# Performance work log

Measured on AMD Instinct MI355X. Metric: run time of the kernel, lower is better.

Reference implementation:

```python
import jax, jax.numpy as jnp
import numpy as np

Q, C, T = 256, 128, 128
L = Q + C + T            # 512
D = 1024                 # d_model
H = 8                    # heads
DK = D // H              # 128 = self_attn.d_k
F = 3                    # num_latent_relations
R = 50                   # num_relation_kinds = len(relations2id)
FF = 4 * D               # feed-forward hidden
DEFAULT_QQ_ID = 0        # relations2id['q:q-default']
EPS = 1e-5


def setup_inputs():
    key = jax.random.key(0)
    ks = jax.random.split(key, 40)
    s = 0.02
    def nrm(k, shape, scale=s):
        return jax.random.normal(k, shape, jnp.float32) * scale
    inp = {
        'x': jax.random.normal(ks[0], (1, L, D), jnp.float32),
        'qc_relation': jax.random.uniform(ks[1], (Q, C, F), jnp.float32),
        'cq_relation': jax.random.uniform(ks[2], (C, Q, F), jnp.float32),
        'qt_relation': jax.random.uniform(ks[3], (Q, T, F), jnp.float32),
        'tq_relation': jax.random.uniform(ks[4], (T, Q, F), jnp.float32),
        'ct_relation': jax.random.randint(ks[5], (C + T, C + T), 0, R, jnp.int32),
        'predefined_relation': jax.random.randint(ks[6], (L, L), 0, R, jnp.int32),
        'mask': jnp.ones((1, L, L), jnp.int32),
        # relation embedding tables
        'rel_k_emb': nrm(ks[7], (R, DK)), 'rel_v_emb': nrm(ks[8], (R, DK)),
        'lqc_k': nrm(ks[9], (F, DK)), 'lqc_v': nrm(ks[10], (F, DK)),
        'lcq_k': nrm(ks[11], (F, DK)), 'lcq_v': nrm(ks[12], (F, DK)),
        'lqt_k': nrm(ks[13], (F, DK)), 'lqt_v': nrm(ks[14], (F, DK)),
        'ltq_k': nrm(ks[15], (F, DK)), 'ltq_v': nrm(ks[16], (F, DK)),
        # attention projections (torch Linear: y = x @ W.T + b)
        'Wq': nrm(ks[17], (D, D)), 'bq': jnp.zeros((D,), jnp.float32),
        'Wk': nrm(ks[18], (D, D)), 'bk': jnp.zeros((D,), jnp.float32),
        'Wv': nrm(ks[19], (D, D)), 'bv': jnp.zeros((D,), jnp.float32),
        'Wo': nrm(ks[20], (D, D)), 'bo': jnp.zeros((D,), jnp.float32),
        # layer norms
        'ln1_g': jnp.ones((D,), jnp.float32), 'ln1_b': jnp.zeros((D,), jnp.float32),
        'ln2_g': jnp.ones((D,), jnp.float32), 'ln2_b': jnp.zeros((D,), jnp.float32),
        # FFN
        'W1': nrm(ks[21], (FF, D)), 'b1': jnp.zeros((FF,), jnp.float32),
        'W2': nrm(ks[22], (D, FF)), 'b2': jnp.zeros((D,), jnp.float32),
    }
    return inp


def layer_norm(x, g, b):
    m = jnp.mean(x, -1, keepdims=True)
    v = jnp.mean((x - m) ** 2, -1, keepdims=True)
    return (x - m) * jax.lax.rsqrt(v + EPS) * g + b


def build_latent_relation(ct, qc, cq, qt, tq, emb, lqc, lcq, lqt, ltq):
    # qq block: every entry is the default-qq embedding row
    qq = jnp.broadcast_to(emb[DEFAULT_QQ_ID], (Q, Q, DK))
    qc_e = jnp.einsum('qcf,fd->qcd', qc, lqc)
    cq_e = jnp.einsum('cqf,fd->cqd', cq, lcq)
    qt_e = jnp.einsum('qtf,fd->qtd', qt, lqt)
    tq_e = jnp.einsum('tqf,fd->tqd', tq, ltq)
    ct_e = emb[ct]                                      # [(c+t),(c+t),DK]
    top = jnp.concatenate([qq, qc_e, qt_e], axis=1)      # [Q, L, DK]
    bot = jnp.concatenate([jnp.concatenate([cq_e, tq_e], 0), ct_e], axis=1)  # [C+T, L, DK]
    return jnp.concatenate([top, bot], axis=0)           # [L, L, DK]


def relation_attention(x, rel_k, rel_v, mask, Wq, bq, Wk, bk, Wv, bv, Wo, bo):
    B = x.shape[0]
    def proj(W, b):
        return (x @ W.T + b).reshape(B, L, H, DK).transpose(0, 2, 1, 3)  # [B,H,L,DK]
    q, k, v = proj(Wq, bq), proj(Wk, bk), proj(Wv, bv)
    scores = (jnp.einsum('bhid,bhjd->bhij', q, k)
              + jnp.einsum('bhid,ijd->bhij', q, rel_k)) / jnp.sqrt(jnp.float32(DK))
    scores = jnp.where(mask[:, None] == 0, jnp.float32(-1e9), scores)
    p = jax.nn.softmax(scores, axis=-1)
    o = (jnp.einsum('bhij,bhjd->bhid', p, v)
         + jnp.einsum('bhij,ijd->bhid', p, rel_v))
    o = o.transpose(0, 2, 1, 3).reshape(B, L, D)
    return o @ Wo.T + bo


def reference(x, qc_relation, cq_relation, qt_relation, tq_relation,
              ct_relation, predefined_relation, mask,
              rel_k_emb, rel_v_emb, lqc_k, lqc_v, lcq_k, lcq_v,
              lqt_k, lqt_v, ltq_k, ltq_v,
              Wq, bq, Wk, bk, Wv, bv, Wo, bo,
              ln1_g, ln1_b, ln2_g, ln2_b, W1, b1, W2, b2):
    # latent relation build + combine with predefined lookup
    rel_k = (rel_k_emb[predefined_relation]
             + build_latent_relation(ct_relation, qc_relation, cq_relation,
                                     qt_relation, tq_relation,
                                     rel_k_emb, lqc_k, lcq_k, lqt_k, ltq_k))
    rel_v = (rel_v_emb[predefined_relation]
             + build_latent_relation(ct_relation, qc_relation, cq_relation,
                                     qt_relation, tq_relation,
                                     rel_v_emb, lqc_v, lcq_v, lqt_v, ltq_v))
    # sublayer 0: pre-norm relation-biased self attention (dropout=0)
    h = x + relation_attention(layer_norm(x, ln1_g, ln1_b), rel_k, rel_v, mask,
                               Wq, bq, Wk, bk, Wv, bv, Wo, bo)
    # sublayer 1: pre-norm FFN
    y = layer_norm(h, ln2_g, ln2_b)
    ffn = jax.nn.relu(y @ W1.T + b1) @ W2.T + b2
    return h + ffn
```

## Files before the change

### kernel.cpp

```cpp
#include <hip/hip_runtime.h>
#include <hip/hip_bf16.h>

#define LL 512
#define DD 1024
#define HH 8
#define DKK 128
#define QQ 256
#define CCC 128
#define TTT 128
#define RR 50
#define FFF 4096
#define KLD 576
#define SLD 576

typedef __attribute__((ext_vector_type(8))) short short8;
typedef __attribute__((ext_vector_type(4))) float float4v;

__device__ __forceinline__ unsigned short f2bu(float f) {
  __hip_bfloat16 h = __float2bfloat16(f);
  unsigned short u; __builtin_memcpy(&u, &h, 2); return u;
}
__device__ __forceinline__ float b2f(unsigned short u) {
  unsigned int v = ((unsigned int)u) << 16;
  float f; __builtin_memcpy(&f, &v, 4); return f;
}
__device__ __forceinline__ int4 cvt8(float4 x, float4 y) {
  int4 o;
  o.x = (int)f2bu(x.x) | ((int)f2bu(x.y) << 16);
  o.y = (int)f2bu(x.z) | ((int)f2bu(x.w) << 16);
  o.z = (int)f2bu(y.x) | ((int)f2bu(y.y) << 16);
  o.w = (int)f2bu(y.z) | ((int)f2bu(y.w) << 16);
  return o;
}

__device__ __forceinline__ void lds_barrier() {
  __builtin_amdgcn_sched_barrier(0);
  __builtin_amdgcn_s_waitcnt(0xC07F);
  __builtin_amdgcn_s_barrier();
  __builtin_amdgcn_sched_barrier(0);
}

#define LOADSET(A0,A1,B0,B1,F0,F1,F2,F3,itv) { int k0v = (itv) << 6;          \
  A0 = *(const int4*)(Az + (size_t)(bm + r)*lda + k0v + gc*8);                \
  A1 = *(const int4*)(Az + (size_t)(bm + 32 + r)*lda + k0v + gc*8);           \
  if constexpr (!CONVB) {                                                     \
    B0 = *(const int4*)(Bz16 + (size_t)(bnb + r)*ldb + k0v + gc*8);           \
    if constexpr (NB > 1)                                                     \
      B1 = *(const int4*)(Bz16 + (size_t)(bnb + 32 + r)*ldb + k0v + gc*8);    \
  } else {                                                                    \
    F0 = *(const float4*)(Bz32 + (size_t)(bnb + r)*ldb + k0v + gc*8);         \
    F1 = *(const float4*)(Bz32 + (size_t)(bnb + r)*ldb + k0v + gc*8 + 4);     \
    if constexpr (NB > 1) {                                                   \
      F2 = *(const float4*)(Bz32 + (size_t)(bnb + 32 + r)*ldb + k0v + gc*8);  \
      F3 = *(const float4*)(Bz32 + (size_t)(bnb + 32 + r)*ldb + k0v + gc*8 + 4); } } }

#define STORESET2(basep,A0,A1,B0,B1,F0,F1,F2,F3) {                            \
  char* bse = (basep);                                                        \
  *(int4*)(bse + r*128 + sl*16) = A0;                                         \
  *(int4*)(bse + (32 + r)*128 + sl*16) = A1;                                  \
  if constexpr (!CONVB) {                                                     \
    *(int4*)(bse + ABYTES + r*128 + sl*16) = B0;                              \
    if constexpr (NB > 1)                                                     \
      *(int4*)(bse + ABYTES + (32 + r)*128 + sl*16) = B1;                     \
  } else {                                                                    \
    *(int4*)(bse + ABYTES + r*128 + sl*16) = cvt8(F0, F1);                    \
    if constexpr (NB > 1)                                                     \
      *(int4*)(bse + ABYTES + (32 + r)*128 + sl*16) = cvt8(F2, F3); } }

__global__ __launch_bounds__(256) void kprep_kernel(
    const float* __restrict__ embk,
    const float* __restrict__ lqc, const float* __restrict__ lqt,
    const float* __restrict__ lcq, const float* __restrict__ ltq,
    unsigned short* __restrict__ Kh)
{
  int g = blockIdx.x*256 + threadIdx.x;
  if (g >= 8*64*128) return;
  int d = g & 127, rr = (g >> 7) & 63, h = g >> 13;
  float v = 0.f;
  if (rr < 50) v = embk[rr*128 + d];
  else if (rr < 62) {
    int u = rr - 50; int tb = u/3, f = u - tb*3;
    const float* tab = (tb==0) ? lqc : (tb==1) ? lqt : (tb==2) ? lcq : ltq;
    v = tab[f*128 + d];
  }
  Kh[((size_t)h*KLD + 512 + rr)*DKK + d] = f2bu(v);
}

__global__ __launch_bounds__(256) void ln_bf16_kernel(const float* __restrict__ x,
    const float* __restrict__ g, const float* __restrict__ b,
    unsigned short* __restrict__ y)
{
  int row = blockIdx.x, t = threadIdx.x;
  const float4 xv = ((const float4*)(x + row*DD))[t];
  float s  = xv.x+xv.y+xv.z+xv.w;
  float ss = xv.x*xv.x+xv.y*xv.y+xv.z*xv.z+xv.w*xv.w;
  __shared__ float rs[256], rss[256];
  rs[t]=s; rss[t]=ss; __syncthreads();
  for (int st=128; st>0; st>>=1){ if (t<st){ rs[t]+=rs[t+st]; rss[t]+=rss[t+st]; } __syncthreads(); }
  float mean = rs[0] * (1.0f/DD);
  float var  = rss[0]*(1.0f/DD) - mean*mean;
  float inv  = rsqrtf(var + 1e-5f);
  float4 gv = ((const float4*)g)[t], bv = ((const float4*)b)[t];
  ushort4 ov;
  ov.x = f2bu((xv.x-mean)*inv*gv.x + bv.x);
  ov.y = f2bu((xv.y-mean)*inv*gv.y + bv.y);
  ov.z = f2bu((xv.z-mean)*inv*gv.z + bv.z);
  ov.w = f2bu((xv.w-mean)*inv*gv.w + bv.w);
  ((ushort4*)(y + row*DD))[t] = ov;
}

__global__ __launch_bounds__(256) void ln_bf16_addb_kernel(float* __restrict__ x,
    const float* __restrict__ g, const float* __restrict__ b,
    const float* __restrict__ b2, unsigned short* __restrict__ y)
{
  int row = blockIdx.x, t = threadIdx.x;
  const float4 xv = ((const float4*)(x + row*DD))[t];
  float s  = xv.x+xv.y+xv.z+xv.w;
  float ss = xv.x*xv.x+xv.y*xv.y+xv.z*xv.z+xv.w*xv.w;
  __shared__ float rs[256], rss[256];
  rs[t]=s; rss[t]=ss; __syncthreads();
  for (int st=128; st>0; st>>=1){ if (t<st){ rs[t]+=rs[t+st]; rss[t]+=rss[t+st]; } __syncthreads(); }
  float mean = rs[0] * (1.0f/DD);
  float var  = rss[0]*(1.0f/DD) - mean*mean;
  float inv  = rsqrtf(var + 1e-5f);
  float4 gv = ((const float4*)g)[t], bv = ((const float4*)b)[t];
  ushort4 ov;
  ov.x = f2bu((xv.x-mean)*inv*gv.x + bv.x);
  ov.y = f2bu((xv.y-mean)*inv*gv.y + bv.y);
  ov.z = f2bu((xv.z-mean)*inv*gv.z + bv.z);
  ov.w = f2bu((xv.w-mean)*inv*gv.w + bv.w);
  ((ushort4*)(y + row*DD))[t] = ov;
  float4 b2v = ((const float4*)b2)[t];
  float4 nx; nx.x = xv.x+b2v.x; nx.y = xv.y+b2v.y; nx.z = xv.z+b2v.z; nx.w = xv.w+b2v.w;
  ((float4*)(x + row*DD))[t] = nx;
}

template<int BN, int DEPTH, int CONVB, int ZK, int OUT_BF16, int RELU, int HAS_SRC, int HAS_BIAS>
__global__ __launch_bounds__(256) void gemm_pl(
    const unsigned short* __restrict__ A, int lda, size_t sAz,
    const void* __restrict__ Bv, int ldb, size_t sBz,
    const float* __restrict__ bias,
    const float* __restrict__ src, int ldsrc, size_t sSz,
    void* __restrict__ Cv, int ldc, size_t sCz,
    int K)
{
  constexpr int BM = 64;
  constexpr int WM = 32, WN = BN/2, FM = 2, FN = WN/16;
  constexpr int NB = BN/32;
  constexpr int ABYTES = BM*128, TILE = ABYTES + BN*128;
  __shared__ char lds[2*TILE];
  int t = threadIdx.x, w = t >> 6, l = t & 63;
  size_t z = blockIdx.z;
  const unsigned short* Az = A + z*sAz;
  const unsigned short* Bz16 = (const unsigned short*)Bv + (CONVB ? 0 : z*sBz);
  const float*          Bz32 = (const float*)Bv + (CONVB ? z*sBz : 0);
  int bm = blockIdx.y*BM, bn = blockIdx.x*BN;
  int bnb = bn;
  int wm = (w>>1)*WM, wn = (w&1)*WN;

  float4v acc[FM][FN];
  #pragma unroll
  for (int m=0;m<FM;++m)
    #pragma unroll
    for (int n=0;n<FN;++n) acc[m][n] = (float4v){0.f,0.f,0.f,0.f};

  int r = t >> 3, sl = t & 7;
  int gc = sl ^ (r & 7);
  int quad = l >> 4, lrow = l & 15;
  const int nit = K >> 6;

  int4 Aa0, Aa1, Ab0, Ab1;  float4 Af0, Af1, Af2, Af3;
  int4 Ba0, Ba1, Bb0, Bb1;  float4 Bf0, Bf1, Bf2, Bf3;
  int4 Ca0, Ca1, Cb0, Cb1;  float4 Cf0, Cf1, Cf2, Cf3;
  int4 Da0, Da1, Db0, Db1;  float4 Df0, Df1, Df2, Df3;

  auto compute = [&](const char* base) {
    const char* ab = base;
    const char* bb = base + ABYTES;
    #pragma unroll
    for (int step=0; step<2; ++step) {
      int c = step*4 + quad;
      short8 af[FM], bf[FN];
      #pragma unroll
      for (int m=0;m<FM;++m) {
        int Rw = wm + m*16 + lrow;
        af[m] = *(const short8*)(ab + Rw*128 + ((c ^ (Rw & 7))*16));
      }
      #pragma unroll
      for (int n=0;n<FN;++n) {
        int Rw = wn + n*16 + lrow;
        bf[n] = *(const short8*)(bb + Rw*128 + ((c ^ (Rw & 7))*16));
      }
      #pragma unroll
      for (int m=0;m<FM;++m)
        #pragma unroll
        for (int n=0;n<FN;++n)
          acc[m][n] = __builtin_amdgcn_mfma_f32_16x16x32_bf16(af[m], bf[n], acc[m][n], 0, 0, 0);
    }
  };

  if constexpr (DEPTH == 2) {
    LOADSET(Aa0,Aa1,Ab0,Ab1,Af0,Af1,Af2,Af3, 0);
    LOADSET(Ba0,Ba1,Bb0,Bb1,Bf0,Bf1,Bf2,Bf3, 1);
    for (int it = 0; it < nit; it += 2) {
      STORESET2(lds, Aa0,Aa1,Ab0,Ab1,Af0,Af1,Af2,Af3);
      if (it + 2 < nit) LOADSET(Aa0,Aa1,Ab0,Ab1,Af0,Af1,Af2,Af3, it+2);
      lds_barrier();
      compute(lds);
      STORESET2(lds + TILE, Ba0,Ba1,Bb0,Bb1,Bf0,Bf1,Bf2,Bf3);
      if (it + 3 < nit) LOADSET(Ba0,Ba1,Bb0,Bb1,Bf0,Bf1,Bf2,Bf3, it+3);
      lds_barrier();
      compute(lds + TILE);
    }
  } else {
    LOADSET(Aa0,Aa1,Ab0,Ab1,Af0,Af1,Af2,Af3, 0);
    LOADSET(Ba0,Ba1,Bb0,Bb1,Bf0,Bf1,Bf2,Bf3, 1);
    LOADSET(Ca0,Ca1,Cb0,Cb1,Cf0,Cf1,Cf2,Cf3, 2);
    LOADSET(Da0,Da1,Db0,Db1,Df0,Df1,Df2,Df3, 3);
    for (int it = 0; it < nit; it += 4) {
      STORESET2(lds, Aa0,Aa1,Ab0,Ab1,Af0,Af1,Af2,Af3);
      if (it + 4 < nit) LOADSET(Aa0,Aa1,Ab0,Ab1,Af0,Af1,Af2,Af3, it+4);
      lds_barrier();
      compute(lds);
      STORESET2(lds + TILE, Ba0,Ba1,Bb0,Bb1,Bf0,Bf1,Bf2,Bf3);
      if (it + 5 < nit) LOADSET(Ba0,Ba1,Bb0,Bb1,Bf0,Bf1,Bf2,Bf3, it+5);
      lds_barrier();
      compute(lds + TILE);
      STORESET2(lds, Ca0,Ca1,Cb0,Cb1,Cf0,Cf1,Cf2,Cf3);
      if (it + 6 < nit) LOADSET(Ca0,Ca1,Cb0,Cb1,Cf0,Cf1,Cf2,Cf3, it+6);
      lds_barrier();
      compute(lds);
      STORESET2(lds + TILE, Da0,Da1,Db0,Db1,Df0,Df1,Df2,Df3);
      if (it + 7 < nit) LOADSET(Da0,Da1,Db0,Db1,Df0,Df1,Df2,Df3, it+7);
      lds_barrier();
      compute(lds + TILE);
    }
  }

  #pragma unroll
  for (int m=0;m<FM;++m)
    #pragma unroll
    for (int n=0;n<FN;++n)
      #pragma unroll
      for (int rg=0;rg<4;++rg) {
        int row = bm + wm + m*16 + quad*4 + rg;
        int col = bn + wn + n*16 + lrow;
        float vv = acc[m][n][rg];
        if (ZK) {
          atomicAdd(&((float*)Cv)[(size_t)row*ldc + col], vv);
        } else {
          if (HAS_BIAS) vv += bias[col];
          if (HAS_SRC)  vv += src[z*sSz + (size_t)row*ldsrc + col];
          if (RELU) vv = fmaxf(vv, 0.f);
          if (OUT_BF16) ((unsigned short*)Cv)[z*sCz + (size_t)row*ldc + col] = f2bu(vv);
          else          ((float*)Cv)[z*sCz + (size_t)row*ldc + col] = vv;
        }
      }
}

__global__ __launch_bounds__(256) void gemm_qkv_pl(
    const unsigned short* __restrict__ A,
    const float* __restrict__ Wq, const float* __restrict__ Wk,
    const float* __restrict__ Wv,
    const float* __restrict__ bq, const float* __restrict__ bk,
    const float* __restrict__ bv,
    unsigned short* __restrict__ Qh, unsigned short* __restrict__ Kh,
    unsigned short* __restrict__ Vt)
{
  constexpr int BN = 64, CONVB = 1;
  constexpr int WM = 32, WN = 32, FM = 2, FN = 2;
  constexpr int NB = 2;
  constexpr int ABYTES = 64*128, TILE = ABYTES + BN*128;
  __shared__ char lds[2*TILE];
  int t = threadIdx.x, w = t >> 6, l = t & 63;
  int bm = blockIdx.y*64, bn = blockIdx.x*BN;
  int wm = (w>>1)*WM, wn = (w&1)*WN;
  const int lda = DD, ldb = DD, nit = DD >> 6;
  const unsigned short* Az = A;
  int part0 = bn >> 10;
  const float* Bz32 = (part0==0 ? Wq : part0==1 ? Wk : Wv) + (size_t)(bn & 1023)*DD;
  const unsigned short* Bz16 = nullptr; (void)Bz16;
  int bnb = 0;

  float4v acc[FM][FN];
  #pragma unroll
  for (int m=0;m<FM;++m)
    #pragma unroll
    for (int n=0;n<FN;++n) acc[m][n] = (float4v){0.f,0.f,0.f,0.f};

  int r = t >> 3, sl = t & 7;
  int gc = sl ^ (r & 7);
  int quad = l >> 4, lrow = l & 15;

  int4 Aa0, Aa1, Ab0, Ab1;  float4 Af0, Af1, Af2, Af3;
  int4 Ba0, Ba1, Bb0, Bb1;  float4 Bf0, Bf1, Bf2, Bf3;
  int4 Ca0, Ca1, Cb0, Cb1;  float4 Cf0, Cf1, Cf2, Cf3;
  int4 Da0, Da1, Db0, Db1;  float4 Df0, Df1, Df2, Df3;

  auto compute = [&](const char* base) {
    const char* ab = base;
    const char* bb = base + ABYTES;
    #pragma unroll
    for (int step=0; step<2; ++step) {
      int c = step*4 + quad;
      short8 af[FM], bf[FN];
      #pragma unroll
      for (int m=0;m<FM;++m) {
        int Rw = wm + m*16 + lrow;
        af[m] = *(const short8*)(ab + Rw*128 + ((c ^ (Rw & 7))*16));
      }
      #pragma unroll
      for (int n=0;n<FN;++n) {
        int Rw = wn + n*16 + lrow;
        bf[n] = *(const short8*)(bb + Rw*128 + ((c ^ (Rw & 7))*16));
      }
      #pragma unroll
      for (int m=0;m<FM;++m)
        #pragma unroll
        for (int n=0;n<FN;++n)
          acc[m][n] = __builtin_amdgcn_mfma_f32_16x16x32_bf16(af[m], bf[n], acc[m][n], 0, 0, 0);
    }
  };

  LOADSET(Aa0,Aa1,Ab0,Ab1,Af0,Af1,Af2,Af3, 0);
  LOADSET(Ba0,Ba1,Bb0,Bb1,Bf0,Bf1,Bf2,Bf3, 1);
  LOADSET(Ca0,Ca1,Cb0,Cb1,Cf0,Cf1,Cf2,Cf3, 2);
  LOADSET(Da0,Da1,Db0,Db1,Df0,Df1,Df2,Df3, 3);
  for (int it = 0; it < nit; it += 4) {
    STORESET2(lds, Aa0,Aa1,Ab0,Ab1,Af0,Af1,Af2,Af3);
    if (it + 4 < nit) LOADSET(Aa0,Aa1,Ab0,Ab1,Af0,Af1,Af2,Af3, it+4);
    lds_barrier();
    compute(lds);
    STORESET2(lds + TILE, Ba0,Ba1,Bb0,Bb1,Bf0,Bf1,Bf2,Bf3);
    if (it + 5 < nit) LOADSET(Ba0,Ba1,Bb0,Bb1,Bf0,Bf1,Bf2,Bf3, it+5);
    lds_barrier();
    compute(lds + TILE);
    STORESET2(lds, Ca0,Ca1,Cb0,Cb1,Cf0,Cf1,Cf2,Cf3);
    if (it + 6 < nit) LOADSET(Ca0,Ca1,Cb0,Cb1,Cf0,Cf1,Cf2,Cf3, it+6);
    lds_barrier();
    compute(lds);
    STORESET2(lds + TILE, Da0,Da1,Db0,Db1,Df0,Df1,Df2,Df3);
    if (it + 7 < nit) LOADSET(Da0,Da1,Db0,Db1,Df0,Df1,Df2,Df3, it+7);
    lds_barrier();
    compute(lds + TILE);
  }

  #pragma unroll
  for (int m=0;m<FM;++m)
    #pragma unroll
    for (int n=0;n<FN;++n)
      #pragma unroll
      for (int rg=0;rg<4;++rg) {
        int row = bm + wm + m*16 + quad*4 + rg;
        int col = bn + wn + n*16 + lrow;
        int part = col >> 10, hh = (col >> 7) & 7, d = col & 127;
        const float* bp = (part==0) ? bq : (part==1) ? bk : bv;
        float vv = acc[m][n][rg] + bp[col & 1023];
        unsigned short o = f2bu(vv);
        if (part == 0)      Qh[((size_t)hh*LL + row)*DKK + d] = o;
        else if (part == 1) Kh[((size_t)hh*KLD + row)*DKK + d] = o;
        else                Vt[((size_t)hh*DKK + d)*LL + row] = o;
      }
}

#define A2_QROWB 272
#define A2_KROWB 272
#define A2_SROWD 586
#define A2_PROWB 1040
#define A2_VROWB 136
#define A2_OFF_KA 2176
#define A2_OFF_KB 19584
#define A2_OFF_S  36992
#define A2_OFF_P  2176
#define A2_OFF_VA 10496
#define A2_OFF_VB 27904
#define A2_OFF_PW 55744
#define A2_OFF_PF1 57408
#define A2_OFF_PF2 57536
#define A2_OFF_SI 57664
#define A2_LDS 57696

__global__ __launch_bounds__(256) void attn_fused(
    const unsigned short* __restrict__ Qh, const unsigned short* __restrict__ Kh,
    const unsigned short* __restrict__ Vt,
    const float* __restrict__ qcr, const float* __restrict__ cqr,
    const float* __restrict__ qtr, const float* __restrict__ tqr,
    const int* __restrict__ ct, const int* __restrict__ pred,
    const int* __restrict__ mask,
    const float* __restrict__ embv, const float* __restrict__ lqc_v,
    const float* __restrict__ lcq_v, const float* __restrict__ lqt_v,
    const float* __restrict__ ltq_v,
    unsigned short* __restrict__ obuf)
{
  __shared__ __align__(16) char lds[A2_LDS];
  const int t = threadIdx.x;
  const int w = t >> 6, l = t & 63, quad = l >> 4, lrow = l & 15;
  const int i0 = blockIdx.x * 8, h = blockIdx.y;

  for (int k2 = t; k2 < 488; k2 += 256) ((float*)(lds + A2_OFF_PW))[k2] = 0.f;

  if (t < 128) {
    int qr = t >> 4, qc = t & 15;
    *(int4*)(lds + qr*A2_QROWB + qc*16) =
        *(const int4*)(Qh + ((size_t)h*LL + i0 + qr)*DKK + qc*8);
  }

  const int kr = t >> 4, kc = t & 15;
  int4 ka0,ka1,ka2,ka3, kb0,kb1,kb2,kb3;

#define A2_LOADKA(jtv) { size_t kb_ = (size_t)h*KLD + (size_t)(jtv)*64 + kr;   \
    ka0 = *(const int4*)(Kh + (kb_     )*DKK + kc*8);                          \
    ka1 = *(const int4*)(Kh + (kb_ + 16)*DKK + kc*8);                          \
    ka2 = *(const int4*)(Kh + (kb_ + 32)*DKK + kc*8);                          \
    ka3 = *(const int4*)(Kh + (kb_ + 48)*DKK + kc*8); }
#define A2_LOADKB(jtv) { size_t kb_ = (size_t)h*KLD + (size_t)(jtv)*64 + kr;   \
    kb0 = *(const int4*)(Kh + (kb_     )*DKK + kc*8);                          \
    kb1 = *(const int4*)(Kh + (kb_ + 16)*DKK + kc*8);                          \
    kb2 = *(const int4*)(Kh + (kb_ + 32)*DKK + kc*8);                          \
    kb3 = *(const int4*)(Kh + (kb_ + 48)*DKK + kc*8); }
#define A2_STOREKA() { char* p_ = lds + A2_OFF_KA;                             \
    *(int4*)(p_ + (kr     )*A2_KROWB + kc*16) = ka0;                           \
    *(int4*)(p_ + (kr + 16)*A2_KROWB + kc*16) = ka1;                           \
    *(int4*)(p_ + (kr + 32)*A2_KROWB + kc*16) = ka2;                           \
    *(int4*)(p_ + (kr + 48)*A2_KROWB + kc*16) = ka3; }
#define A2_STOREKB() { char* p_ = lds + A2_OFF_KB;                             \
    *(int4*)(p_ + (kr     )*A2_KROWB + kc*16) = kb0;                           \
    *(int4*)(p_ + (kr + 16)*A2_KROWB + kc*16) = kb1;                           \
    *(int4*)(p_ + (kr + 32)*A2_KROWB + kc*16) = kb2;                           \
    *(int4*)(p_ + (kr + 48)*A2_KROWB + kc*16) = kb3; }

  auto qk_tile = [&](const char* kb, int jt) {
    float4v acc = (float4v){0.f,0.f,0.f,0.f};
    #pragma unroll
    for (int kk = 0; kk < 4; ++kk) {
      int c = kk*4 + quad;
      short8 af = *(const short8*)(lds + lrow*A2_QROWB + c*16);
      short8 bf = *(const short8*)(kb + (w*16 + lrow)*A2_KROWB + c*16);
      acc = __builtin_amdgcn_mfma_f32_16x16x32_bf16(af, bf, acc, 0, 0, 0);
    }
    if (quad < 2) {
      #pragma unroll
      for (int rg = 0; rg < 4; ++rg)
        ((float*)(lds + A2_OFF_S))[(quad*4 + rg)*A2_SROWD + jt*64 + w*16 + lrow] = acc[rg];
    }
  };

  A2_LOADKA(0); A2_LOADKB(1);
  A2_STOREKA(); A2_LOADKA(2); lds_barrier(); qk_tile(lds + A2_OFF_KA, 0);
  A2_STOREKB(); A2_LOADKB(3); lds_barrier(); qk_tile(lds + A2_OFF_KB, 1);
  A2_STOREKA(); A2_LOADKA(4); lds_barrier(); qk_tile(lds + A2_OFF_KA, 2);
  A2_STOREKB(); A2_LOADKB(5); lds_barrier(); qk_tile(lds + A2_OFF_KB, 3);
  A2_STOREKA(); A2_LOADKA(6); lds_barrier(); qk_tile(lds + A2_OFF_KA, 4);
  A2_STOREKB(); A2_LOADKB(7); lds_barrier(); qk_tile(lds + A2_OFF_KB, 5);
  A2_STOREKA(); A2_LOADKA(8); lds_barrier(); qk_tile(lds + A2_OFF_KA, 6);
  A2_STOREKB();               lds_barrier(); qk_tile(lds + A2_OFF_KB, 7);
  A2_STOREKA();               lds_barrier(); qk_tile(lds + A2_OFF_KA, 8);
  lds_barrier();

  const int row = t >> 5, l32 = t & 31;
  const int i = i0 + row;
  const float* Sp = (const float*)(lds + A2_OFF_S) + row*A2_SROWD;
  const int bse = (i0 < QQ) ? 562 : (i0 < QQ + CCC) ? 568 : 571;
  const float lq1a = Sp[bse], lq1b = Sp[bse+1], lq1c = Sp[bse+2];
  const float lq2a = Sp[565], lq2b = Sp[566], lq2c = Sp[567];

  const int vr = t >> 3, vc = t & 7;
  int4 va0,va1,va2,va3, vb0,vb1,vb2,vb3;
#define A2_LOADVA(itv) { size_t vb_ = (size_t)h*DKK + vr;                      \
    size_t vo_ = (size_t)(itv)*64 + vc*8;                                      \
    va0 = *(const int4*)(Vt + (vb_      )*LL + vo_);                           \
    va1 = *(const int4*)(Vt + (vb_ + 32)*LL + vo_);                            \
    va2 = *(const int4*)(Vt + (vb_ + 64)*LL + vo_);                            \
    va3 = *(const int4*)(Vt + (vb_ + 96)*LL + vo_); }
#define A2_LOADVB(itv) { size_t vb_ = (size_t)h*DKK + vr;                      \
    size_t vo_ = (size_t)(itv)*64 + vc*8;                                      \
    vb0 = *(const int4*)(Vt + (vb_      )*LL + vo_);                           \
    vb1 = *(const int4*)(Vt + (vb_ + 32)*LL + vo_);                            \
    vb2 = *(const int4*)(Vt + (vb_ + 64)*LL + vo_);                            \
    vb3 = *(const int4*)(Vt + (vb_ + 96)*LL + vo_); }
#define A2_STOREVA() { char* p_ = lds + A2_OFF_VA;                             \
    *(int4*)(p_ + (vr     )*A2_VROWB + vc*16) = va0;                           \
    *(int4*)(p_ + (vr + 32)*A2_VROWB + vc*16) = va1;                           \
    *(int4*)(p_ + (vr + 64)*A2_VROWB + vc*16) = va2;                           \
    *(int4*)(p_ + (vr + 96)*A2_VROWB + vc*16) = va3; }
#define A2_STOREVB() { char* p_ = lds + A2_OFF_VB;                             \
    *(int4*)(p_ + (vr     )*A2_VROWB + vc*16) = vb0;                           \
    *(int4*)(p_ + (vr + 32)*A2_VROWB + vc*16) = vb1;                           \
    *(int4*)(p_ + (vr + 64)*A2_VROWB + vc*16) = vb2;                           \
    *(int4*)(p_ + (vr + 96)*A2_VROWB + vc*16) = vb3; }

  A2_LOADVA(0); A2_LOADVB(1);

  float sum=0.f, f0=0.f, f1=0.f, f2=0.f, g0=0.f, g1=0.f, g2=0.f;
  float* pwsrow = (float*)(lds + A2_OFF_PW) + row*52;
  #pragma unroll
  for (int m = 0; m < 16; ++m) {
    int j = m*32 + l32;
    int predv = pred[i*LL + j];
    int maskv = mask[i*LL + j];
    float s = Sp[j] + Sp[512 + predv];
    float c0=0.f, c1=0.f, c2=0.f; int rt; int scat2 = 0;
    if (i0 < QQ) {
      if (j < QQ) { s += Sp[512]; rt = 0; }
      else if (j < QQ + CCC) {
        const float* r3 = qcr + ((size_t)i*CCC + (j - QQ))*3;
        c0 = r3[0]; c1 = r3[1]; c2 = r3[2];
        s += c0*lq1a + c1*lq1b + c2*lq1c; rt = 1;
      } else {
        const float* r3 = qtr + ((size_t)i*TTT + (j - QQ - CCC))*3;
        c0 = r3[0]; c1 = r3[1]; c2 = r3[2];
        s += c0*lq2a + c1*lq2b + c2*lq2c; rt = 2;
      }
    } else {
      if (j < QQ) {
        const float* r3 = (i < QQ + CCC) ? cqr + ((size_t)(i - QQ)*QQ + j)*3
                                         : tqr + ((size_t)(i - QQ - CCC)*QQ + j)*3;
        c0 = r3[0]; c1 = r3[1]; c2 = r3[2];
        s += c0*lq1a + c1*lq1b + c2*lq1c; rt = 1;
      } else {
        scat2 = ct[(i - QQ)*(CCC + TTT) + (j - QQ)];
        s += Sp[512 + scat2]; rt = 0;
      }
    }
    s *= 0.08838834764831845f;
    float e = (maskv == 0) ? 0.f : __expf(s);
    sum += e;
    *(unsigned short*)(lds + A2_OFF_P + row*A2_PROWB + j*2) = f2bu(e);
    atomicAdd(pwsrow + predv, e);
    if (rt == 0)      atomicAdd(pwsrow + scat2, e);
    else if (rt == 1) { f0 += e*c0; f1 += e*c1; f2 += e*c2; }
    else              { g0 += e*c0; g1 += e*c1; g2 += e*c2; }
  }
  #pragma unroll
  for (int off = 16; off >= 1; off >>= 1) {
    sum += __shfl_xor(sum, off);
    f0 += __shfl_xor(f0, off); f1 += __shfl_xor(f1, off); f2 += __shfl_xor(f2, off);
    g0 += __shfl_xor(g0, off); g1 += __shfl_xor(g1, off); g2 += __shfl_xor(g2, off);
  }
  if (l32 == 0) {
    float* pf1 = (float*)(lds + A2_OFF_PF1) + row*4;
    float* pf2 = (float*)(lds + A2_OFF_PF2) + row*4;
    pf1[0] = f0; pf1[1] = f1; pf1[2] = f2;
    pf2[0] = g0; pf2[1] = g1; pf2[2] = g2;
    ((float*)(lds + A2_OFF_SI))[row] = 1.0f / sum;
  }

  float4v oacc0 = (float4v){0.f,0.f,0.f,0.f};
  float4v oacc1 = (float4v){0.f,0.f,0.f,0.f};
  auto pv_tile = [&](const char* vbase, int it) {
    #pragma unroll
    for (int kk = 0; kk < 2; ++kk) {
      int c = kk*4 + quad;
      short8 pa  = *(const short8*)(lds + A2_OFF_P + lrow*A2_PROWB + it*128 + c*16);
      short8 vf0 = *(const short8*)(vbase + (w*32 + lrow)*A2_VROWB + c*16);
      short8 vf1 = *(const short8*)(vbase + (w*32 + 16 + lrow)*A2_VROWB + c*16);
      oacc0 = __builtin_amdgcn_mfma_f32_16x16x32_bf16(pa, vf0, oacc0, 0, 0, 0);
      oacc1 = __builtin_amdgcn_mfma_f32_16x16x32_bf16(pa, vf1, oacc1, 0, 0, 0);
    }
  };
  A2_STOREVA(); A2_LOADVA(2); lds_barrier(); pv_tile(lds + A2_OFF_VA, 0);
  A2_STOREVB(); A2_LOADVB(3); lds_barrier(); pv_tile(lds + A2_OFF_VB, 1);
  A2_STOREVA(); A2_LOADVA(4); lds_barrier(); pv_tile(lds + A2_OFF_VA, 2);
  A2_STOREVB(); A2_LOADVB(5); lds_barrier(); pv_tile(lds + A2_OFF_VB, 3);
  A2_STOREVA(); A2_LOADVA(6); lds_barrier(); pv_tile(lds + A2_OFF_VA, 4);
  A2_STOREVB(); A2_LOADVB(7); lds_barrier(); pv_tile(lds + A2_OFF_VB, 5);
  A2_STOREVA();               lds_barrier(); pv_tile(lds + A2_OFF_VA, 6);
  A2_STOREVB();               lds_barrier(); pv_tile(lds + A2_OFF_VB, 7);

  if (quad < 2) {
    const float* tab1 = (i0 < QQ) ? lqc_v : (i0 < QQ + CCC) ? lcq_v : ltq_v;
    const bool hasT2 = (i0 < QQ);
    const float* pws = (const float*)(lds + A2_OFF_PW);
    const float* sinv = (const float*)(lds + A2_OFF_SI);
    #pragma unroll
    for (int n = 0; n < 2; ++n) {
      int d = w*32 + n*16 + lrow;
      float a0=0.f, a1=0.f, a2=0.f, a3=0.f;
      #pragma unroll 5
      for (int rr = 0; rr < RR; ++rr) {
        float evv = embv[rr*DKK + d];
        a0 += pws[(quad*4+0)*52 + rr]*evv;
        a1 += pws[(quad*4+1)*52 + rr]*evv;
        a2 += pws[(quad*4+2)*52 + rr]*evv;
        a3 += pws[(quad*4+3)*52 + rr]*evv;
      }
      float t0 = tab1[d], t1 = tab1[DKK + d], t2 = tab1[2*DKK + d];
      float u0 = 0.f, u1 = 0.f, u2 = 0.f;
      if (hasT2) { u0 = lqt_v[d]; u1 = lqt_v[DKK + d]; u2 = lqt_v[2*DKK + d]; }
      #pragma unroll
      for (int rg = 0; rg < 4; ++rg) {
        int rw = quad*4 + rg;
        const float* pf1 = (const float*)(lds + A2_OFF_PF1) + rw*4;
        const float* pf2 = (const float*)(lds + A2_OFF_PF2) + rw*4;
        float aval = (rg==0) ? a0 : (rg==1) ? a1 : (rg==2) ? a2 : a3;
        float oval = (n==0) ? oacc0[rg] : oacc1[rg];
        float val = (oval + aval
                  + pf1[0]*t0 + pf1[1]*t1 + pf1[2]*t2
                  + pf2[0]*u0 + pf2[1]*u1 + pf2[2]*u2) * sinv[rw];
        obuf[(size_t)(i0 + rw)*DD + h*DKK + d] = f2bu(val);
      }
    }
  }
}

extern "C" void kernel_launch(void* const* d_in, const int* in_sizes, int n_in,
                              void* d_out, int out_size, void* d_ws, size_t ws_size,
                              hipStream_t stream)
{
  const float* x    = (const float*)d_in[0];
  const float* qcr  = (const float*)d_in[1];
  const float* cqr  = (const float*)d_in[2];
  const float* qtr  = (const float*)d_in[3];
  const float* tqr  = (const float*)d_in[4];
  const int*   ct   = (const int*)d_in[5];
  const int*   pred = (const int*)d_in[6];
  const int*   mask = (const int*)d_in[7];
  const float* embk = (const float*)d_in[8];
  const float* embv = (const float*)d_in[9];
  const float* lqc_k = (const float*)d_in[10];
  const float* lqc_v = (const float*)d_in[11];
  const float* lcq_k = (const float*)d_in[12];
  const float* lcq_v = (const float*)d_in[13];
  const float* lqt_k = (const float*)d_in[14];
  const float* lqt_v = (const float*)d_in[15];
  const float* ltq_k = (const float*)d_in[16];
  const float* ltq_v = (const float*)d_in[17];
  const float* Wq = (const float*)d_in[18]; const float* bq = (const float*)d_in[19];
  const float* Wk = (const float*)d_in[20]; const float* bk = (const float*)d_in[21];
  const float* Wv = (const float*)d_in[22]; const float* bv = (const float*)d_in[23];
  const float* Wo = (const float*)d_in[24]; const float* bo = (const float*)d_in[25];
  const float* ln1_g = (const float*)d_in[26]; const float* ln1_b = (const float*)d_in[27];
  const float* ln2_g = (const float*)d_in[28]; const float* ln2_b = (const float*)d_in[29];
  const float* W1 = (const float*)d_in[30]; const float* b1 = (const float*)d_in[31];
  const float* W2 = (const float*)d_in[32]; const float* b2 = (const float*)d_in[33];
  float* out = (float*)d_out;

  float* wsf = (float*)d_ws;
  float* S    = wsf;
  float* o2   = S + (size_t)HH*LL*SLD;
  unsigned short* ub = (unsigned short*)(o2 + (size_t)HH*LL*DKK);
  unsigned short* ybuf_b = ub;
  unsigned short* obuf_b = ybuf_b + LL*DD;
  unsigned short* Qh     = obuf_b + LL*DD;
  unsigned short* Kh     = Qh + (size_t)HH*LL*DKK;
  unsigned short* Vt     = Kh + (size_t)HH*KLD*DKK;
  unsigned short* hidden = (unsigned short*)S;

  kprep_kernel<<<(8*64*128 + 255)/256, 256, 0, stream>>>(
      embk, lqc_k, lqt_k, lcq_k, ltq_k, Kh);
  ln_bf16_kernel<<<LL, 256, 0, stream>>>(x, ln1_g, ln1_b, ybuf_b);
  gemm_qkv_pl<<<dim3(48, 8), 256, 0, stream>>>(ybuf_b, Wq, Wk, Wv, bq, bk, bv,
                                               Qh, Kh, Vt);
  attn_fused<<<dim3(64, 8), 256, 0, stream>>>(
      Qh, Kh, Vt, qcr, cqr, qtr, tqr, ct, pred, mask,
      embv, lqc_v, lcq_v, lqt_v, ltq_v, obuf_b);
  gemm_pl<32,4,1,0,0,0,1,1><<<dim3(32, 8, 1), 256, 0, stream>>>(
      obuf_b, DD, 0, Wo, DD, 0, bo, x, DD, 0, out, DD, 0, DD);
  ln_bf16_addb_kernel<<<LL, 256, 0, stream>>>(out, ln2_g, ln2_b, b2, ybuf_b);
  gemm_pl<64,4,1,0,1,1,0,1><<<dim3(64, 8, 1), 256, 0, stream>>>(
      ybuf_b, DD, 0, W1, DD, 0, b1, nullptr, 0, 0, hidden, FFF, 0, DD);
  gemm_pl<64,4,1,1,0,0,0,0><<<dim3(16, 8, 4), 256, 0, stream>>>(
      hidden, FFF, (size_t)1024, W2, FFF, (size_t)1024,
      nullptr, nullptr, 0, 0, out, DD, 0, 1024);
}
```

Measured before the change: 247.3 us.

## Store K/V in MFMA-fragment-friendly layout and load fragments directly from global

```diff
diff --git a/kernel.cpp b/kernel.cpp
--- a/kernel.cpp
+++ b/kernel.cpp
@@ -66,6 +66,7 @@
     *(int4*)(bse + ABYTES + r*128 + sl*16) = cvt8(F0, F1);                    \
     if constexpr (NB > 1)                                                     \
       *(int4*)(bse + ABYTES + (32 + r)*128 + sl*16) = cvt8(F2, F3); } }
+
 
 __global__ __launch_bounds__(256) void kprep_kernel(
     const float* __restrict__ embk,
@@ -83,7 +84,7 @@
     const float* tab = (tb==0) ? lqc : (tb==1) ? lqt : (tb==2) ? lcq : ltq;
     v = tab[f*128 + d];
   }
-  Kh[((size_t)h*KLD + 512 + rr)*DKK + d] = f2bu(v);
+  Kh[(((size_t)h*16 + (d>>3))*KLD + 512 + rr)*8 + (d&7)] = f2bu(v);
 }
 
 __global__ __launch_bounds__(256) void ln_bf16_kernel(const float* __restrict__ x,
@@ -358,27 +359,23 @@
         float vv = acc[m][n][rg] + bp[col & 1023];
         unsigned short o = f2bu(vv);
         if (part == 0)      Qh[((size_t)hh*LL + row)*DKK + d] = o;
-        else if (part == 1) Kh[((size_t)hh*KLD + row)*DKK + d] = o;
-        else                Vt[((size_t)hh*DKK + d)*LL + row] = o;
-      }
-}
-
-#define A2_QROWB 272
-#define A2_KROWB 272
-#define A2_SROWD 586
-#define A2_PROWB 1040
-#define A2_VROWB 136
-#define A2_OFF_KA 2176
-#define A2_OFF_KB 19584
-#define A2_OFF_S  36992
-#define A2_OFF_P  2176
-#define A2_OFF_VA 10496
-#define A2_OFF_VB 27904
-#define A2_OFF_PW 55744
-#define A2_OFF_PF1 57408
-#define A2_OFF_PF2 57536
-#define A2_OFF_SI 57664
-#define A2_LDS 57696
+        else if (part == 1) Kh[(((size_t)hh*16 + (d>>3))*KLD + row)*8 + (d&7)] = o;
+        else                Vt[(((size_t)hh*64 + (row>>3))*128 + d)*8 + (row&7)] = o;
+      }
+}
+
+#define A3_QROWB 272
+#define A3_PROWB 1040
+#define A3_SROWD 584
+#define A3_O2ROW 132
+#define A3_OFF_P   2176
+#define A3_OFF_S   10496
+#define A3_OFF_PW  29184
+#define A3_OFF_PF1 30848
+#define A3_OFF_PF2 30976
+#define A3_OFF_SI  31104
+#define A3_OFF_O2  31136
+#define A3_LDS     35360
 
 __global__ __launch_bounds__(256) void attn_fused(
     const unsigned short* __restrict__ Qh, const unsigned short* __restrict__ Kh,
@@ -392,107 +389,56 @@
     const float* __restrict__ ltq_v,
     unsigned short* __restrict__ obuf)
 {
-  __shared__ __align__(16) char lds[A2_LDS];
+  __shared__ __align__(16) char lds[A3_LDS];
   const int t = threadIdx.x;
   const int w = t >> 6, l = t & 63, quad = l >> 4, lrow = l & 15;
   const int i0 = blockIdx.x * 8, h = blockIdx.y;
 
-  for (int k2 = t; k2 < 488; k2 += 256) ((float*)(lds + A2_OFF_PW))[k2] = 0.f;
+  for (int k2 = t; k2 < 488; k2 += 256) ((float*)(lds + A3_OFF_PW))[k2] = 0.f;
 
   if (t < 128) {
     int qr = t >> 4, qc = t & 15;
-    *(int4*)(lds + qr*A2_QROWB + qc*16) =
+    *(int4*)(lds + qr*A3_QROWB + qc*16) =
         *(const int4*)(Qh + ((size_t)h*LL + i0 + qr)*DKK + qc*8);
   }
-
-  const int kr = t >> 4, kc = t & 15;
-  int4 ka0,ka1,ka2,ka3, kb0,kb1,kb2,kb3;
-
-#define A2_LOADKA(jtv) { size_t kb_ = (size_t)h*KLD + (size_t)(jtv)*64 + kr;   \
-    ka0 = *(const int4*)(Kh + (kb_     )*DKK + kc*8);                          \
-    ka1 = *(const int4*)(Kh + (kb_ + 16)*DKK + kc*8);                          \
-    ka2 = *(const int4*)(Kh + (kb_ + 32)*DKK + kc*8);                          \
-    ka3 = *(const int4*)(Kh + (kb_ + 48)*DKK + kc*8); }
-#define A2_LOADKB(jtv) { size_t kb_ = (size_t)h*KLD + (size_t)(jtv)*64 + kr;   \
-    kb0 = *(const int4*)(Kh + (kb_     )*DKK + kc*8);                          \
-    kb1 = *(const int4*)(Kh + (kb_ + 16)*DKK + kc*8);                          \
-    kb2 = *(const int4*)(Kh + (kb_ + 32)*DKK + kc*8);                          \
-    kb3 = *(const int4*)(Kh + (kb_ + 48)*DKK + kc*8); }
-#define A2_STOREKA() { char* p_ = lds + A2_OFF_KA;                             \
-    *(int4*)(p_ + (kr     )*A2_KROWB + kc*16) = ka0;                           \
-    *(int4*)(p_ + (kr + 16)*A2_KROWB + kc*16) = ka1;                           \
-    *(int4*)(p_ + (kr + 32)*A2_KROWB + kc*16) = ka2;                           \
-    *(int4*)(p_ + (kr + 48)*A2_KROWB + kc*16) = ka3; }
-#define A2_STOREKB() { char* p_ = lds + A2_OFF_KB;                             \
-    *(int4*)(p_ + (kr     )*A2_KROWB + kc*16) = kb0;                           \
-    *(int4*)(p_ + (kr + 16)*A2_KROWB + kc*16) = kb1;                           \
-    *(int4*)(p_ + (kr + 32)*A2_KROWB + kc*16) = kb2;                           \
-    *(int4*)(p_ + (kr + 48)*A2_KROWB + kc*16) = kb3; }
-
-  auto qk_tile = [&](const char* kb, int jt) {
-    float4v acc = (float4v){0.f,0.f,0.f,0.f};
-    #pragma unroll
-    for (int kk = 0; kk < 4; ++kk) {
-      int c = kk*4 + quad;
-      short8 af = *(const short8*)(lds + lrow*A2_QROWB + c*16);
-      short8 bf = *(const short8*)(kb + (w*16 + lrow)*A2_KROWB + c*16);
-      acc = __builtin_amdgcn_mfma_f32_16x16x32_bf16(af, bf, acc, 0, 0, 0);
-    }
-    if (quad < 2) {
-      #pragma unroll
-      for (int rg = 0; rg < 4; ++rg)
-        ((float*)(lds + A2_OFF_S))[(quad*4 + rg)*A2_SROWD + jt*64 + w*16 + lrow] = acc[rg];
-    }
-  };
-
-  A2_LOADKA(0); A2_LOADKB(1);
-  A2_STOREKA(); A2_LOADKA(2); lds_barrier(); qk_tile(lds + A2_OFF_KA, 0);
-  A2_STOREKB(); A2_LOADKB(3); lds_barrier(); qk_tile(lds + A2_OFF_KB, 1);
-  A2_STOREKA(); A2_LOADKA(4); lds_barrier(); qk_tile(lds + A2_OFF_KA, 2);
-  A2_STOREKB(); A2_LOADKB(5); lds_barrier(); qk_tile(lds + A2_OFF_KB, 3);
-  A2_STOREKA(); A2_LOADKA(6); lds_barrier(); qk_tile(lds + A2_OFF_KA, 4);
-  A2_STOREKB(); A2_LOADKB(7); lds_barrier(); qk_tile(lds + A2_OFF_KB, 5);
-  A2_STOREKA(); A2_LOADKA(8); lds_barrier(); qk_tile(lds + A2_OFF_KA, 6);
-  A2_STOREKB();               lds_barrier(); qk_tile(lds + A2_OFF_KB, 7);
-  A2_STOREKA();               lds_barrier(); qk_tile(lds + A2_OFF_KA, 8);
+  lds_barrier();
+
+  {
+    const unsigned short* Kc = Kh + (size_t)h*16*KLD*8;
+    short8 af0 = *(const short8*)(lds + lrow*A3_QROWB + (quad     )*16);
+    short8 af1 = *(const short8*)(lds + lrow*A3_QROWB + (quad +  4)*16);
+    short8 af2 = *(const short8*)(lds + lrow*A3_QROWB + (quad +  8)*16);
+    short8 af3 = *(const short8*)(lds + lrow*A3_QROWB + (quad + 12)*16);
+    #pragma unroll
+    for (int jt = 0; jt < 9; ++jt) {
+      float4v acc = (float4v){0.f,0.f,0.f,0.f};
+      int krow = jt*64 + w*16 + lrow;
+      short8 bf0 = *(const short8*)(Kc + ((size_t)(quad     )*KLD + krow)*8);
+      short8 bf1 = *(const short8*)(Kc + ((size_t)(quad +  4)*KLD + krow)*8);
+      short8 bf2 = *(const short8*)(Kc + ((size_t)(quad +  8)*KLD + krow)*8);
+      short8 bf3 = *(const short8*)(Kc + ((size_t)(quad + 12)*KLD + krow)*8);
+      acc = __builtin_amdgcn_mfma_f32_16x16x32_bf16(af0, bf0, acc, 0, 0, 0);
+      acc = __builtin_amdgcn_mfma_f32_16x16x32_bf16(af1, bf1, acc, 0, 0, 0);
+      acc = __builtin_amdgcn_mfma_f32_16x16x32_bf16(af2, bf2, acc, 0, 0, 0);
+      acc = __builtin_amdgcn_mfma_f32_16x16x32_bf16(af3, bf3, acc, 0, 0, 0);
+      if (quad < 2) {
+        #pragma unroll
+        for (int rg = 0; rg < 4; ++rg)
+          ((float*)(lds + A3_OFF_S))[(quad*4 + rg)*A3_SROWD + jt*64 + w*16 + lrow] = acc[rg];
+      }
+    }
+  }
   lds_barrier();
 
   const int row = t >> 5, l32 = t & 31;
   const int i = i0 + row;
-  const float* Sp = (const float*)(lds + A2_OFF_S) + row*A2_SROWD;
+  const float* Sp = (const float*)(lds + A3_OFF_S) + row*A3_SROWD;
   const int bse = (i0 < QQ) ? 562 : (i0 < QQ + CCC) ? 568 : 571;
   const float lq1a = Sp[bse], lq1b = Sp[bse+1], lq1c = Sp[bse+2];
   const float lq2a = Sp[565], lq2b = Sp[566], lq2c = Sp[567];
 
-  const int vr = t >> 3, vc = t & 7;
-  int4 va0,va1,va2,va3, vb0,vb1,vb2,vb3;
-#define A2_LOADVA(itv) { size_t vb_ = (size_t)h*DKK + vr;                      \
-    size_t vo_ = (size_t)(itv)*64 + vc*8;                                      \
-    va0 = *(const int4*)(Vt + (vb_      )*LL + vo_);                           \
-    va1 = *(const int4*)(Vt + (vb_ + 32)*LL + vo_);                            \
-    va2 = *(const int4*)(Vt + (vb_ + 64)*LL + vo_);                            \
-    va3 = *(const int4*)(Vt + (vb_ + 96)*LL + vo_); }
-#define A2_LOADVB(itv) { size_t vb_ = (size_t)h*DKK + vr;                      \
-    size_t vo_ = (size_t)(itv)*64 + vc*8;                                      \
-    vb0 = *(const int4*)(Vt + (vb_      )*LL + vo_);                           \
-    vb1 = *(const int4*)(Vt + (vb_ + 32)*LL + vo_);                            \
-    vb2 = *(const int4*)(Vt + (vb_ + 64)*LL + vo_);                            \
-    vb3 = *(const int4*)(Vt + (vb_ + 96)*LL + vo_); }
-#define A2_STOREVA() { char* p_ = lds + A2_OFF_VA;                             \
-    *(int4*)(p_ + (vr     )*A2_VROWB + vc*16) = va0;                           \
-    *(int4*)(p_ + (vr + 32)*A2_VROWB + vc*16) = va1;                           \
-    *(int4*)(p_ + (vr + 64)*A2_VROWB + vc*16) = va2;                           \
-    *(int4*)(p_ + (vr + 96)*A2_VROWB + vc*16) = va3; }
-#define A2_STOREVB() { char* p_ = lds + A2_OFF_VB;                             \
-    *(int4*)(p_ + (vr     )*A2_VROWB + vc*16) = vb0;                           \
-    *(int4*)(p_ + (vr + 32)*A2_VROWB + vc*16) = vb1;                           \
-    *(int4*)(p_ + (vr + 64)*A2_VROWB + vc*16) = vb2;                           \
-    *(int4*)(p_ + (vr + 96)*A2_VROWB + vc*16) = vb3; }
-
-  A2_LOADVA(0); A2_LOADVB(1);
-
   float sum=0.f, f0=0.f, f1=0.f, f2=0.f, g0=0.f, g1=0.f, g2=0.f;
-  float* pwsrow = (float*)(lds + A2_OFF_PW) + row*52;
+  float* pwsrow = (float*)(lds + A3_OFF_PW) + row*52;
   #pragma unroll
   for (int m = 0; m < 16; ++m) {
     int j = m*32 + l32;
@@ -525,7 +471,7 @@
     s *= 0.08838834764831845f;
     float e = (maskv == 0) ? 0.f : __expf(s);
     sum += e;
-    *(unsigned short*)(lds + A2_OFF_P + row*A2_PROWB + j*2) = f2bu(e);
+    *(unsigned short*)(lds + A3_OFF_P + row*A3_PROWB + j*2) = f2bu(e);
     atomicAdd(pwsrow + predv, e);
     if (rt == 0)      atomicAdd(pwsrow + scat2, e);
     else if (rt == 1) { f0 += e*c0; f1 += e*c1; f2 += e*c2; }
@@ -538,65 +484,77 @@
     g0 += __shfl_xor(g0, off); g1 += __shfl_xor(g1, off); g2 += __shfl_xor(g2, off);
   }
   if (l32 == 0) {
-    float* pf1 = (float*)(lds + A2_OFF_PF1) + row*4;
-    float* pf2 = (float*)(lds + A2_OFF_PF2) + row*4;
+    float* pf1 = (float*)(lds + A3_OFF_PF1) + row*4;
+    float* pf2 = (float*)(lds + A3_OFF_PF2) + row*4;
     pf1[0] = f0; pf1[1] = f1; pf1[2] = f2;
     pf2[0] = g0; pf2[1] = g1; pf2[2] = g2;
-    ((float*)(lds + A2_OFF_SI))[row] = 1.0f / sum;
-  }
+    ((float*)(lds + A3_OFF_SI))[row] = 1.0f / sum;
+  }
+  lds_barrier();
+
+  {
+    int orow = t >> 5, d0 = (t & 31)*4;
+    const float* pwsr = (const float*)(lds + A3_OFF_PW) + orow*52;
+    float a0=0.f, a1=0.f, a2=0.f, a3=0.f;
+    #pragma unroll 5
+    for (int rr = 0; rr < RR; ++rr) {
+      float pv = pwsr[rr];
+      float4 ev = *(const float4*)(embv + rr*DKK + d0);
+      a0 += pv*ev.x; a1 += pv*ev.y; a2 += pv*ev.z; a3 += pv*ev.w;
+    }
+    const float* tab1 = (i0 < QQ) ? lqc_v : (i0 < QQ + CCC) ? lcq_v : ltq_v;
+    const float* pf1 = (const float*)(lds + A3_OFF_PF1) + orow*4;
+    float4 t0 = *(const float4*)(tab1 + d0);
+    float4 t1 = *(const float4*)(tab1 + DKK + d0);
+    float4 t2 = *(const float4*)(tab1 + 2*DKK + d0);
+    a0 += pf1[0]*t0.x + pf1[1]*t1.x + pf1[2]*t2.x;
+    a1 += pf1[0]*t0.y + pf1[1]*t1.y + pf1[2]*t2.y;
+    a2 += pf1[0]*t0.z + pf1[1]*t1.z + pf1[2]*t2.z;
+    a3 += pf1[0]*t0.w + pf1[1]*t1.w + pf1[2]*t2.w;
+    if (i0 < QQ) {
+      const float* pf2 = (const float*)(lds + A3_OFF_PF2) + orow*4;
+      float4 u0 = *(const float4*)(lqt_v + d0);
+      float4 u1 = *(const float4*)(lqt_v + DKK + d0);
+      float4 u2 = *(const float4*)(lqt_v + 2*DKK + d0);
+      a0 += pf2[0]*u0.x + pf2[1]*u1.x + pf2[2]*u2.x;
+      a1 += pf2[0]*u0.y + pf2[1]*u1.y + pf2[2]*u2.y;
+      a2 += pf2[0]*u0.z + pf2[1]*u1.z + pf2[2]*u2.z;
+      a3 += pf2[0]*u0.w + pf2[1]*u1.w + pf2[2]*u2.w;
+    }
+    float4 av; av.x=a0; av.y=a1; av.z=a2; av.w=a3;
+    *(float4*)((float*)(lds + A3_OFF_O2) + orow*A3_O2ROW + d0) = av;
+  }
+  lds_barrier();
 
   float4v oacc0 = (float4v){0.f,0.f,0.f,0.f};
   float4v oacc1 = (float4v){0.f,0.f,0.f,0.f};
-  auto pv_tile = [&](const char* vbase, int it) {
-    #pragma unroll
-    for (int kk = 0; kk < 2; ++kk) {
-      int c = kk*4 + quad;
-      short8 pa  = *(const short8*)(lds + A2_OFF_P + lrow*A2_PROWB + it*128 + c*16);
-      short8 vf0 = *(const short8*)(vbase + (w*32 + lrow)*A2_VROWB + c*16);
-      short8 vf1 = *(const short8*)(vbase + (w*32 + 16 + lrow)*A2_VROWB + c*16);
-      oacc0 = __builtin_amdgcn_mfma_f32_16x16x32_bf16(pa, vf0, oacc0, 0, 0, 0);
-      oacc1 = __builtin_amdgcn_mfma_f32_16x16x32_bf16(pa, vf1, oacc1, 0, 0, 0);
-    }
-  };
-  A2_STOREVA(); A2_LOADVA(2); lds_barrier(); pv_tile(lds + A2_OFF_VA, 0);
-  A2_STOREVB(); A2_LOADVB(3); lds_barrier(); pv_tile(lds + A2_OFF_VB, 1);
-  A2_STOREVA(); A2_LOADVA(4); lds_barrier(); pv_tile(lds + A2_OFF_VA, 2);
-  A2_STOREVB(); A2_LOADVB(5); lds_barrier(); pv_tile(lds + A2_OFF_VB, 3);
-  A2_STOREVA(); A2_LOADVA(6); lds_barrier(); pv_tile(lds + A2_OFF_VA, 4);
-  A2_STOREVB(); A2_LOADVB(7); lds_barrier(); pv_tile(lds + A2_OFF_VB, 5);
-  A2_STOREVA();               lds_barrier(); pv_tile(lds + A2_OFF_VA, 6);
-  A2_STOREVB();               lds_barrier(); pv_tile(lds + A2_OFF_VB, 7);
+  {
+    const unsigned short* Vc = Vt + (size_t)h*64*128*8;
+    #pragma unroll
+    for (int it = 0; it < 8; ++it) {
+      #pragma unroll
+      for (int kk = 0; kk < 2; ++kk) {
+        int c = kk*4 + quad;
+        short8 pa  = *(const short8*)(lds + A3_OFF_P + lrow*A3_PROWB + it*128 + c*16);
+        short8 vf0 = *(const short8*)(Vc + (((size_t)(it*8 + c))*128 + w*32 + lrow)*8);
+        short8 vf1 = *(const short8*)(Vc + (((size_t)(it*8 + c))*128 + w*32 + 16 + lrow)*8);
+        oacc0 = __builtin_amdgcn_mfma_f32_16x16x32_bf16(pa, vf0, oacc0, 0, 0, 0);
+        oacc1 = __builtin_amdgcn_mfma_f32_16x16x32_bf16(pa, vf1, oacc1, 0, 0, 0);
+      }
+    }
+  }
 
   if (quad < 2) {
-    const float* tab1 = (i0 < QQ) ? lqc_v : (i0 < QQ + CCC) ? lcq_v : ltq_v;
-    const bool hasT2 = (i0 < QQ);
-    const float* pws = (const float*)(lds + A2_OFF_PW);
-    const float* sinv = (const float*)(lds + A2_OFF_SI);
+    const float* o2s = (const float*)(lds + A3_OFF_O2);
+    const float* sinv = (const float*)(lds + A3_OFF_SI);
     #pragma unroll
     for (int n = 0; n < 2; ++n) {
       int d = w*32 + n*16 + lrow;
-      float a0=0.f, a1=0.f, a2=0.f, a3=0.f;
-      #pragma unroll 5
-      for (int rr = 0; rr < RR; ++rr) {
-        float evv = embv[rr*DKK + d];
-        a0 += pws[(quad*4+0)*52 + rr]*evv;
-        a1 += pws[(quad*4+1)*52 + rr]*evv;
-        a2 += pws[(quad*4+2)*52 + rr]*evv;
-        a3 += pws[(quad*4+3)*52 + rr]*evv;
-      }
-      float t0 = tab1[d], t1 = tab1[DKK + d], t2 = tab1[2*DKK + d];
-      float u0 = 0.f, u1 = 0.f, u2 = 0.f;
-      if (hasT2) { u0 = lqt_v[d]; u1 = lqt_v[DKK + d]; u2 = lqt_v[2*DKK + d]; }
       #pragma unroll
       for (int rg = 0; rg < 4; ++rg) {
         int rw = quad*4 + rg;
-        const float* pf1 = (const float*)(lds + A2_OFF_PF1) + rw*4;
-        const float* pf2 = (const float*)(lds + A2_OFF_PF2) + rw*4;
-        float aval = (rg==0) ? a0 : (rg==1) ? a1 : (rg==2) ? a2 : a3;
         float oval = (n==0) ? oacc0[rg] : oacc1[rg];
-        float val = (oval + aval
-                  + pf1[0]*t0 + pf1[1]*t1 + pf1[2]*t2
-                  + pf2[0]*u0 + pf2[1]*u1 + pf2[2]*u2) * sinv[rw];
+        float val = (oval + o2s[rw*A3_O2ROW + d]) * sinv[rw];
         obuf[(size_t)(i0 + rw)*DD + h*DKK + d] = f2bu(val);
       }
     }
```

New measurement: 235.9 us. -4.6%, faster.
